# Kernel optimization log

Measured on AMD Instinct MI355X. Metric: run time of the kernel, lower is better.

Reference implementation:

```python
import jax, jax.numpy as jnp
import numpy as np

B, T_V, T_A = 128, 64, 128
E_V, E_A = 1024, 512
H, EMB, C = 1024, 512, 512  # C = input_size - embedding_size
IN = EMB + C               # RNN input size = 1024
VOCAB = 20000


def setup_inputs() -> dict:
    key = jax.random.key(0)
    ks = jax.random.split(key, 26)
    s = 0.02
    inp = {
        "input": jax.random.normal(ks[0], (B, 1, EMB), jnp.float32),
        "enc_visual": jax.random.normal(ks[1], (B, T_V, E_V), jnp.float32),
        "enc_audio": jax.random.normal(ks[2], (B, T_A, E_A), jnp.float32),
        "hidden_state": jax.random.normal(ks[3], (1, B, H), jnp.float32),
        "cell_state": jax.random.normal(ks[4], (1, B, H), jnp.float32),
        # visual attention (Bahdanau): W1:[C,H], W2:[C,E_V], W3:[1,C]
        "W_va1": s * jax.random.normal(ks[5], (C, H), jnp.float32),
        "W_va2": s * jax.random.normal(ks[6], (C, E_V), jnp.float32),
        "W_va3": s * jax.random.normal(ks[7], (1, C), jnp.float32),
        "W_venc": s * jax.random.normal(ks[8], (C, E_V), jnp.float32),
        # audio attention
        "W_aa1": s * jax.random.normal(ks[9], (C, H), jnp.float32),
        "W_aa2": s * jax.random.normal(ks[10], (C, E_A), jnp.float32),
        "W_aa3": s * jax.random.normal(ks[11], (1, C), jnp.float32),
        "W_aenc": s * jax.random.normal(ks[12], (C, E_A), jnp.float32),
        # cross-modal context attention (over 2 context vectors)
        "W_ca1": s * jax.random.normal(ks[13], (C, H), jnp.float32),
        "W_ca2": s * jax.random.normal(ks[14], (C, C), jnp.float32),
        "W_ca3": s * jax.random.normal(ks[15], (1, C), jnp.float32),
        # LSTM-style custom RNN cell params
        "W_ih": s * jax.random.normal(ks[16], (4 * H, IN), jnp.float32),
        "W_hh": s * jax.random.normal(ks[17], (4 * H, H), jnp.float32),
        "b_ih": jnp.zeros((4 * H,), jnp.float32),
        "b_hh": jnp.zeros((4 * H,), jnp.float32),
        # output projection
        "W_out": s * jax.random.normal(ks[18], (VOCAB, H), jnp.float32),
        "b_out": jnp.zeros((VOCAB,), jnp.float32),
    }
    return inp


def _attend(h, enc, W1, W2, W3):
    # h: [B,H]; enc: [B,T,E]. Vectorized Bahdanau attention (original loops over T).
    v1 = h @ W1.T                               # [B,C]
    v2 = jnp.einsum('bte,ce->btc', enc, W2)     # [B,T,C]
    scores = jnp.tanh(v1[:, None, :] + v2) @ W3.T  # [B,T,1]
    attn = jax.nn.softmax(scores[..., 0], axis=1)  # [B,T]
    return jnp.einsum('bt,bte->be', attn, enc)     # [B,E]


def reference(input, enc_visual, enc_audio, hidden_state, cell_state,
              W_va1, W_va2, W_va3, W_venc,
              W_aa1, W_aa2, W_aa3, W_aenc,
              W_ca1, W_ca2, W_ca3,
              W_ih, W_hh, b_ih, b_hh, W_out, b_out):
    h0 = hidden_state[0]   # [B,H]
    c0 = cell_state[0]     # [B,H]

    vc = _attend(h0, enc_visual, W_va1, W_va2, W_va3) @ W_venc.T  # [B,C]
    ac = _attend(h0, enc_audio, W_aa1, W_aa2, W_aa3) @ W_aenc.T   # [B,C]
    all_ctx = jnp.stack([vc, ac], axis=1)                         # [B,2,C]
    final_ctx = _attend(h0, all_ctx, W_ca1, W_ca2, W_ca3)         # [B,C]

    x = jnp.concatenate([input[:, 0, :], jnp.tanh(final_ctx)], axis=-1)  # [B,IN]
    gates = x @ W_ih.T + b_ih + h0 @ W_hh.T + b_hh                 # [B,4H]
    i, f, g, o = jnp.split(gates, 4, axis=-1)
    c_new = jax.nn.sigmoid(f) * c0 + jax.nn.sigmoid(i) * jnp.tanh(g)
    h_new = jax.nn.sigmoid(o) * jnp.tanh(c_new)

    logits = h_new @ W_out.T + b_out                               # [B,V]
    return (logits[:, None, :], h_new[None], c_new[None])
```

## Files before the change

kernel.cpp:

```cpp
#include <hip/hip_runtime.h>
#include <hip/hip_bf16.h>
#include <cstddef>

typedef __attribute__((ext_vector_type(8))) short short8;
typedef __attribute__((ext_vector_type(4))) float f32x4;

static __device__ __forceinline__ f32x4 ldg(const float* p) {
    return *(const f32x4*)p;
}

static __device__ __forceinline__ short8 pack8(f32x4 f0, f32x4 f1) {
    union { __hip_bfloat162 h[4]; short8 s; } u;
    u.h[0] = __float22bfloat162_rn(make_float2(f0.x, f0.y));
    u.h[1] = __float22bfloat162_rn(make_float2(f0.z, f0.w));
    u.h[2] = __float22bfloat162_rn(make_float2(f1.x, f1.y));
    u.h[3] = __float22bfloat162_rn(make_float2(f1.z, f1.w));
    return u.s;
}

static __device__ __forceinline__ void gload16(const short* g, short* l) {
    __builtin_amdgcn_global_load_lds(
        (const __attribute__((address_space(1))) void*)g,
        (__attribute__((address_space(3))) void*)l, 16, 0, 0);
}

static __device__ __forceinline__ void lds_barrier() {
    asm volatile("s_waitcnt lgkmcnt(0)" ::: "memory");
    __builtin_amdgcn_s_barrier();
    asm volatile("" ::: "memory");
}

static __device__ __forceinline__ void sk_body(
    const float* __restrict__ A, int lda,
    const float* __restrict__ W,
    const float* __restrict__ bias, int addbias,
    float* __restrict__ C, int ldc, int N,
    int kbeg, int kend, int n0, int m0)
{
    __shared__ short As[2][128 * 32];
    __shared__ short Ws[2][64 * 32];
    const int tid  = threadIdx.x;
    const int lane = tid & 63;
    const int wave = tid >> 6;
    const int wm = wave * 32;

    f32x4 acc[2][4];
    #pragma unroll
    for (int i = 0; i < 2; ++i)
        #pragma unroll
        for (int j = 0; j < 4; ++j)
            acc[i][j] = (f32x4){0.f, 0.f, 0.f, 0.f};

    const int arow = tid >> 1;
    const int ah   = tid & 1;
    const int afs  = (arow >> 1) & 3;
    const float* gA = A + (size_t)(m0 + arow) * lda + kbeg + ah * 16;
    const int aoff0 = arow * 32 + (((ah * 2)     ^ afs) * 8);
    const int aoff1 = arow * 32 + (((ah * 2 + 1) ^ afs) * 8);

    const int wrow  = tid >> 2;
    const int wslot = tid & 3;
    const int wvalid = (n0 + wrow) < N;
    const float* gW = W + (size_t)(n0 + wrow) * lda + kbeg + wslot * 8;
    const int woff = wrow * 32 + ((wslot ^ ((wrow >> 1) & 3)) * 8);

    const int frow = lane & 15;
    const int hi   = lane >> 4;
    const int fsl  = (hi ^ ((frow >> 1) & 3)) * 8;
    const int ra   = (wm + frow) * 32 + fsl;
    const int rb   = frow * 32 + fsl;

    const int nsteps = (kend - kbeg) >> 5;

    f32x4 a0_[4], a1_[4], w0_[2], w1_[2];
    #pragma unroll
    for (int q = 0; q < 4; ++q) a0_[q] = ldg(gA + q * 4);
    #pragma unroll
    for (int q = 0; q < 4; ++q) a1_[q] = ldg(gA + 32 + q * 4);
    if (wvalid) {
        w0_[0] = ldg(gW);      w0_[1] = ldg(gW + 4);
        w1_[0] = ldg(gW + 32); w1_[1] = ldg(gW + 36);
    } else {
        w0_[0] = w0_[1] = w1_[0] = w1_[1] = (f32x4){0.f, 0.f, 0.f, 0.f};
    }

    for (int s = 0; s < nsteps; s += 2) {
        {
            short* as = As[0]; short* ws = Ws[0];
            *(short8*)(as + aoff0) = pack8(a0_[0], a0_[1]);
            *(short8*)(as + aoff1) = pack8(a0_[2], a0_[3]);
            *(short8*)(ws + woff)  = pack8(w0_[0], w0_[1]);
            if (s + 2 < nsteps) {
                const float* nA = gA + (s + 2) * 32;
                #pragma unroll
                for (int q = 0; q < 4; ++q) a0_[q] = ldg(nA + q * 4);
                if (wvalid) {
                    const float* nW = gW + (s + 2) * 32;
                    w0_[0] = ldg(nW); w0_[1] = ldg(nW + 4);
                }
            }
            lds_barrier();
            short8 af[2], bf[4];
            #pragma unroll
            for (int i = 0; i < 2; ++i) af[i] = *(const short8*)(as + ra + i * 512);
            #pragma unroll
            for (int j = 0; j < 4; ++j) bf[j] = *(const short8*)(ws + rb + j * 512);
            #pragma unroll
            for (int i = 0; i < 2; ++i)
                #pragma unroll
                for (int j = 0; j < 4; ++j)
                    acc[i][j] = __builtin_amdgcn_mfma_f32_16x16x32_bf16(af[i], bf[j], acc[i][j], 0, 0, 0);
        }
        {
            short* as = As[1]; short* ws = Ws[1];
            *(short8*)(as + aoff0) = pack8(a1_[0], a1_[1]);
            *(short8*)(as + aoff1) = pack8(a1_[2], a1_[3]);
            *(short8*)(ws + woff)  = pack8(w1_[0], w1_[1]);
            if (s + 3 < nsteps) {
                const float* nA = gA + (s + 3) * 32;
                #pragma unroll
                for (int q = 0; q < 4; ++q) a1_[q] = ldg(nA + q * 4);
                if (wvalid) {
                    const float* nW = gW + (s + 3) * 32;
                    w1_[0] = ldg(nW); w1_[1] = ldg(nW + 4);
                }
            }
            lds_barrier();
            short8 af[2], bf[4];
            #pragma unroll
            for (int i = 0; i < 2; ++i) af[i] = *(const short8*)(as + ra + i * 512);
            #pragma unroll
            for (int j = 0; j < 4; ++j) bf[j] = *(const short8*)(ws + rb + j * 512);
            #pragma unroll
            for (int i = 0; i < 2; ++i)
                #pragma unroll
                for (int j = 0; j < 4; ++j)
                    acc[i][j] = __builtin_amdgcn_mfma_f32_16x16x32_bf16(af[i], bf[j], acc[i][j], 0, 0, 0);
        }
    }

    const int cl = lane & 15;
    const int rq = hi * 4;
    #pragma unroll
    for (int j = 0; j < 4; ++j) {
        int gc = n0 + j * 16 + cl;
        if (gc >= N) continue;
        float b = addbias ? bias[gc] : 0.f;
        #pragma unroll
        for (int i = 0; i < 2; ++i) {
            int gr = m0 + wm + i * 16 + rq;
            #pragma unroll
            for (int r = 0; r < 4; ++r)
                atomicAdd(C + (size_t)(gr + r) * ldc + gc, acc[i][j][r] + b);
        }
    }
}

__global__ __launch_bounds__(256) void gemm_sk(
    const float* __restrict__ A, const float* __restrict__ W,
    const float* __restrict__ bias, float* __restrict__ C,
    int N, int K, int kchunk, int ldc)
{
    int kbeg = blockIdx.y * kchunk;
    sk_body(A, K, W, bias, bias != nullptr && blockIdx.y == 0,
            C, ldc, N, kbeg, kbeg + kchunk, blockIdx.x * 64, blockIdx.z * 128);
}

__global__ __launch_bounds__(256) void hproj3_mfma(
    const float* __restrict__ h0,
    const float* __restrict__ Wa, const float* __restrict__ Wb, const float* __restrict__ Wc,
    float* __restrict__ hbase)
{
    int n0g = blockIdx.x * 64;
    int wsel = n0g >> 9;
    const float* W = (wsel == 0) ? Wa : (wsel == 1) ? Wb : Wc;
    float* C = hbase + (size_t)wsel * 128 * 512;
    int kbeg = blockIdx.y * 128;
    sk_body(h0, 1024, W, nullptr, 0, C, 512, 512, kbeg, kbeg + 128, n0g & 511, 0);
}

__global__ __launch_bounds__(256) void ctxproj_mfma(
    const float* __restrict__ attv, const float* __restrict__ Wv,
    const float* __restrict__ atta, const float* __restrict__ Wa,
    float* __restrict__ ctx)
{
    const float* A; const float* W; float* C; int lda, kb, ke;
    if (blockIdx.z == 0) { A = attv; W = Wv; C = ctx;       lda = 1024; kb = blockIdx.y * 128; ke = kb + 128; }
    else                 { A = atta; W = Wa; C = ctx + 512; lda = 512;  kb = blockIdx.y * 64;  ke = kb + 64;  }
    sk_body(A, lda, W, nullptr, 0, C, 1024, 512, kb, ke, blockIdx.x * 64, 0);
}

__global__ __launch_bounds__(256) void gates_mfma(
    const float* __restrict__ xb, const float* __restrict__ W_ih,
    const float* __restrict__ h0, const float* __restrict__ W_hh,
    float* __restrict__ gates)
{
    int pair = blockIdx.y >> 2;
    const float* A = pair ? h0 : xb;
    const float* W = pair ? W_hh : W_ih;
    int kb = (blockIdx.y & 3) * 256;
    sk_body(A, 1024, W, nullptr, 0, gates, 4096, 4096, kb, kb + 256, blockIdx.x * 64, 0);
}

__global__ __launch_bounds__(256) void cvt_bf16(
    const float* __restrict__ encv, const float* __restrict__ enca,
    const float* __restrict__ wv2,  const float* __restrict__ wa2,
    short* __restrict__ oev, short* __restrict__ oea,
    short* __restrict__ owv, short* __restrict__ owa)
{
    int bid = blockIdx.x;
    const float* src; short* dst; int lb;
    if (bid < 4096)      { src = encv; dst = oev; lb = bid; }
    else if (bid < 8192) { src = enca; dst = oea; lb = bid - 4096; }
    else if (bid < 8448) { src = wv2;  dst = owv; lb = bid - 8192; }
    else                 { src = wa2;  dst = owa; lb = bid - 8448; }
    size_t off = ((size_t)lb * 256 + threadIdx.x) * 8;
    f32x4 f0 = *(const f32x4*)(src + off);
    f32x4 f1 = *(const f32x4*)(src + off + 4);
    *(short8*)(dst + off) = pack8(f0, f1);
}

__global__ __launch_bounds__(256) void scores_fused(
    const short* __restrict__ Av, const short* __restrict__ Wv,
    const float* __restrict__ hv1,  const float* __restrict__ W_va3,
    float* __restrict__ scv,
    const short* __restrict__ Aa, const short* __restrict__ Wa,
    const float* __restrict__ ha1,  const float* __restrict__ W_aa3,
    float* __restrict__ sca)
{
    __shared__ short As[2][4096];
    __shared__ short Ws[2][4096];

    const short *A, *W; const float *v1, *W3;
    float* sc;
    int K, tshift, n0, m0;
    int idx = blockIdx.x;
    if (idx < 256) {
        n0 = (idx >> 6) * 128;  m0 = (idx & 63) * 128;
        A = Av; W = Wv; v1 = hv1; W3 = W_va3; sc = scv;
        K = 1024; tshift = 6;
    } else {
        idx -= 256;
        n0 = (idx >> 7) * 128;  m0 = (idx & 127) * 128;
        A = Aa; W = Wa; v1 = ha1; W3 = W_aa3; sc = sca;
        K = 512; tshift = 7;
    }

    const int tid  = threadIdx.x;
    const int lane = tid & 63;
    const int wave = tid >> 6;
    const int wr = wave >> 1;
    const int wc = wave & 1;

    f32x4 acc[4][4];
    #pragma unroll
    for (int i = 0; i < 4; ++i)
        #pragma unroll
        for (int j = 0; j < 4; ++j)
            acc[i][j] = (f32x4){0.f, 0.f, 0.f, 0.f};

    const int srow = lane >> 2;
    const int slsw = (lane & 3) ^ ((lane >> 3) & 3);
    const short* gA0 = A + (size_t)(m0 + wave * 16 + srow) * K + slsw * 8;
    const short* gA1 = gA0 + (size_t)64 * K;
    const short* gW0 = W + (size_t)(n0 + wave * 16 + srow) * K + slsw * 8;
    const short* gW1 = gW0 + (size_t)64 * K;
    const int ldsw = wave * 512;

    const int frow = lane & 15;
    const int hi   = lane >> 4;
    const int fsl  = (hi ^ ((frow >> 1) & 3)) * 8;
    const int raBase = (wr * 64 + frow) * 32 + fsl;
    const int rbBase = (wc * 64 + frow) * 32 + fsl;

    const int nsteps = K >> 5;

    gload16(gA0, As[0] + ldsw);
    gload16(gA1, As[0] + 2048 + ldsw);
    gload16(gW0, Ws[0] + ldsw);
    gload16(gW1, Ws[0] + 2048 + ldsw);

    int cur = 0;
    for (int s = 0; s < nsteps; ++s) {
        int nk = (s + 1 < nsteps ? s + 1 : s) * 32;
        gload16(gA0 + nk, As[cur ^ 1] + ldsw);
        gload16(gA1 + nk, As[cur ^ 1] + 2048 + ldsw);
        gload16(gW0 + nk, Ws[cur ^ 1] + ldsw);
        gload16(gW1 + nk, Ws[cur ^ 1] + 2048 + ldsw);
        asm volatile("s_waitcnt vmcnt(4)" ::: "memory");
        __builtin_amdgcn_s_barrier();
        __builtin_amdgcn_sched_barrier(0);

        const short* as = As[cur];
        const short* ws = Ws[cur];
        short8 af[4], bf[4];
        #pragma unroll
        for (int i = 0; i < 4; ++i) af[i] = *(const short8*)(as + raBase + i * 512);
        #pragma unroll
        for (int j = 0; j < 4; ++j) bf[j] = *(const short8*)(ws + rbBase + j * 512);
        #pragma unroll
        for (int i = 0; i < 4; ++i)
            #pragma unroll
            for (int j = 0; j < 4; ++j)
                acc[i][j] = __builtin_amdgcn_mfma_f32_16x16x32_bf16(af[i], bf[j], acc[i][j], 0, 0, 0);
        __builtin_amdgcn_sched_barrier(0);
        __builtin_amdgcn_s_barrier();
        cur ^= 1;
    }

    const int cl = lane & 15;
    const int rq = hi * 4;
    #pragma unroll
    for (int i = 0; i < 4; ++i) {
        #pragma unroll
        for (int r = 0; r < 4; ++r) {
            int gr = m0 + wr * 64 + i * 16 + rq + r;
            const float* v1row = v1 + (size_t)(gr >> tshift) * 512;
            float p = 0.f;
            #pragma unroll
            for (int j = 0; j < 4; ++j) {
                int gc = n0 + wc * 64 + j * 16 + cl;
                p += tanhf(v1row[gc] + acc[i][j][r]) * W3[gc];
            }
            p += __shfl_xor(p, 1, 64);
            p += __shfl_xor(p, 2, 64);
            p += __shfl_xor(p, 4, 64);
            p += __shfl_xor(p, 8, 64);
            if (cl == 0) atomicAdd(sc + gr, p);
        }
    }
}

__global__ __launch_bounds__(256) void attend_out2(
    const float* __restrict__ scv, const float* __restrict__ encv, float* __restrict__ attv,
    const float* __restrict__ sca, const float* __restrict__ enca, float* __restrict__ atta)
{
    const float* sc; const float* enc; float* out;
    int T, E, ec;
    if (blockIdx.y < 4) { sc = scv; enc = encv; out = attv; T = 64;  E = 1024; ec = blockIdx.y; }
    else                { sc = sca; enc = enca; out = atta; T = 128; E = 512;  ec = blockIdx.y - 4; }

    __shared__ float ew[128];
    const int b = blockIdx.x, tid = threadIdx.x;
    __shared__ float raw[128];
    if (tid < T) raw[tid] = sc[(size_t)b * T + tid];
    __syncthreads();
    float m = -1e30f;
    for (int t = 0; t < T; ++t) m = fmaxf(m, raw[t]);
    if (tid < T) ew[tid] = __expf(raw[tid] - m);
    __syncthreads();
    float sum = 0.f;
    for (int t = 0; t < T; ++t) sum += ew[t];
    const float inv = 1.f / sum;

    const int e = ec * 256 + tid;
    const float* encb = enc + (size_t)b * T * E + e;
    float acc = 0.f;
    for (int t = 0; t < T; ++t)
        acc += ew[t] * encb[(size_t)t * E];
    out[(size_t)b * E + e] = acc * inv;
}

__global__ __launch_bounds__(256) void cross_kernel(
    const float* __restrict__ hc1, const float* __restrict__ v2c,
    const float* __restrict__ W3, const float* __restrict__ ctx,
    const float* __restrict__ inp, float* __restrict__ x)
{
    const int C = 512;
    __shared__ float red[256];
    __shared__ float aw[2];
    const int b = blockIdx.x, tid = threadIdx.x;

    float p0 = 0.f, p1 = 0.f;
    for (int c = tid; c < C; c += 256) {
        float h = hc1[(size_t)b * C + c], w = W3[c];
        p0 += tanhf(h + v2c[(size_t)(b * 2 + 0) * C + c]) * w;
        p1 += tanhf(h + v2c[(size_t)(b * 2 + 1) * C + c]) * w;
    }
    red[tid] = p0; __syncthreads();
    for (int s = 128; s; s >>= 1) { if (tid < s) red[tid] += red[tid + s]; __syncthreads(); }
    float s0 = red[0];
    __syncthreads();
    red[tid] = p1; __syncthreads();
    for (int s = 128; s; s >>= 1) { if (tid < s) red[tid] += red[tid + s]; __syncthreads(); }
    if (tid == 0) {
        float s1 = red[0];
        float m = fmaxf(s0, s1);
        float e0 = __expf(s0 - m), e1 = __expf(s1 - m);
        float inv = 1.f / (e0 + e1);
        aw[0] = e0 * inv; aw[1] = e1 * inv;
    }
    __syncthreads();
    float a0 = aw[0], a1 = aw[1];
    for (int c = tid; c < C; c += 256) {
        float fc = a0 * ctx[(size_t)(b * 2 + 0) * C + c]
                 + a1 * ctx[(size_t)(b * 2 + 1) * C + c];
        x[(size_t)b * 1024 + 512 + c] = tanhf(fc);
        x[(size_t)b * 1024 + c] = inp[(size_t)b * 512 + c];
    }
}

__global__ __launch_bounds__(256) void lstm_kernel(
    const float* __restrict__ gates, const float* __restrict__ c0,
    const float* __restrict__ b_ih, const float* __restrict__ b_hh,
    float* __restrict__ hout, float* __restrict__ cout)
{
    const int idx = blockIdx.x * 256 + threadIdx.x;
    const int b = idx >> 10, h = idx & 1023;
    const float* g = gates + (size_t)b * 4096;
    float gi = g[h]        + b_ih[h]        + b_hh[h];
    float gf = g[1024 + h] + b_ih[1024 + h] + b_hh[1024 + h];
    float gg = g[2048 + h] + b_ih[2048 + h] + b_hh[2048 + h];
    float go = g[3072 + h] + b_ih[3072 + h] + b_hh[3072 + h];
    float si = 1.f / (1.f + __expf(-gi));
    float sf = 1.f / (1.f + __expf(-gf));
    float so = 1.f / (1.f + __expf(-go));
    float cn = sf * c0[idx] + si * tanhf(gg);
    float hn = so * tanhf(cn);
    cout[idx] = cn;
    hout[idx] = hn;
}

extern "C" void kernel_launch(void* const* d_in, const int* in_sizes, int n_in,
                              void* d_out, int out_size, void* d_ws, size_t ws_size,
                              hipStream_t stream)
{
    const float* inp    = (const float*)d_in[0];
    const float* encv   = (const float*)d_in[1];
    const float* enca   = (const float*)d_in[2];
    const float* h0     = (const float*)d_in[3];
    const float* c0     = (const float*)d_in[4];
    const float* W_va1  = (const float*)d_in[5];
    const float* W_va2  = (const float*)d_in[6];
    const float* W_va3  = (const float*)d_in[7];
    const float* W_venc = (const float*)d_in[8];
    const float* W_aa1  = (const float*)d_in[9];
    const float* W_aa2  = (const float*)d_in[10];
    const float* W_aa3  = (const float*)d_in[11];
    const float* W_aenc = (const float*)d_in[12];
    const float* W_ca1  = (const float*)d_in[13];
    const float* W_ca2  = (const float*)d_in[14];
    const float* W_ca3  = (const float*)d_in[15];
    const float* W_ih   = (const float*)d_in[16];
    const float* W_hh   = (const float*)d_in[17];
    const float* b_ih   = (const float*)d_in[18];
    const float* b_hh   = (const float*)d_in[19];
    const float* W_out  = (const float*)d_in[20];
    const float* b_out  = (const float*)d_in[21];
    float* out = (float*)d_out;

    float* ws = (float*)d_ws;
    float* hv1  = ws;  ws += 128 * 512;
    float* ha1  = ws;  ws += 128 * 512;
    float* hc1  = ws;  ws += 128 * 512;
    float* scv  = ws;  ws += 128 * 64;
    float* sca  = ws;  ws += 128 * 128;
    float* ctx  = ws;  ws += 128 * 2 * 512;
    float* v2c  = ws;  ws += 128 * 2 * 512;
    float* gates= ws;  ws += (size_t)128 * 4096;
    size_t zero_floats = (size_t)(ws - (float*)d_ws);
    float* xb   = ws;  ws += 128 * 1024;
    float* attv = ws;  ws += 128 * 1024;
    float* atta = ws;  ws += 128 * 512;
    short* encv_bf = (short*)ws;  ws += 8388608 / 2;
    short* enca_bf = (short*)ws;  ws += 8388608 / 2;
    short* wv2_bf  = (short*)ws;  ws += 524288 / 2;
    short* wa2_bf  = (short*)ws;  ws += 262144 / 2;

    dim3 blk(256);

    hipMemsetAsync(d_ws, 0, zero_floats * sizeof(float), stream);
    hipMemsetAsync(out, 0, (size_t)128 * 20000 * sizeof(float), stream);

    cvt_bf16<<<dim3(8576), blk, 0, stream>>>(encv, enca, W_va2, W_aa2,
                                             encv_bf, enca_bf, wv2_bf, wa2_bf);
    hproj3_mfma<<<dim3(24, 8), blk, 0, stream>>>(h0, W_va1, W_aa1, W_ca1, hv1);
    scores_fused<<<dim3(768), blk, 0, stream>>>(encv_bf, wv2_bf, hv1, W_va3, scv,
                                                enca_bf, wa2_bf, ha1, W_aa3, sca);
    attend_out2<<<dim3(128, 6), blk, 0, stream>>>(scv, encv, attv, sca, enca, atta);
    ctxproj_mfma<<<dim3(8, 8, 2), blk, 0, stream>>>(attv, W_venc, atta, W_aenc, ctx);
    gemm_sk<<<dim3(8, 4, 2), blk, 0, stream>>>(ctx, W_ca2, nullptr, v2c, 512, 512, 128, 512);
    cross_kernel<<<128, blk, 0, stream>>>(hc1, v2c, W_ca3, ctx, inp, xb);
    gates_mfma<<<dim3(64, 8), blk, 0, stream>>>(xb, W_ih, h0, W_hh, gates);
    float* hout = out + 2560000;
    float* cout = out + 2560000 + 131072;
    lstm_kernel<<<512, blk, 0, stream>>>(gates, c0, b_ih, b_hh, hout, cout);
    gemm_sk<<<dim3(313, 2, 1), blk, 0, stream>>>(hout, W_out, b_out, out, 20000, 1024, 512, 20000);
}
```

Baseline: 374.6 us.

## Use async global-to-LDS fp32 loads in split-K GEMM and bf16 encoder reads in attention

The split-K GEMM body now stages fp32 A and W tiles directly into LDS with global_load_lds, double-buffered with vmcnt waits. It converts to bf16 while reading fragments from LDS, where before it loaded into registers and packed before storing. Separately, the attention-output kernel reads the bf16 copies of the encoder outputs instead of fp32, halving its traffic and the block count. Risks are higher LDS usage (fp32 tiles), bf16 precision in the weighted sum, and the W row clamping used for out-of-range rows in place of zero fill.

Result: no change. 381.8 us (+1.9%).

```diff
diff --git a/kernel.cpp b/kernel.cpp
--- a/kernel.cpp
+++ b/kernel.cpp
@@ -4,10 +4,6 @@
 
 typedef __attribute__((ext_vector_type(8))) short short8;
 typedef __attribute__((ext_vector_type(4))) float f32x4;
-
-static __device__ __forceinline__ f32x4 ldg(const float* p) {
-    return *(const f32x4*)p;
-}
 
 static __device__ __forceinline__ short8 pack8(f32x4 f0, f32x4 f1) {
     union { __hip_bfloat162 h[4]; short8 s; } u;
@@ -23,11 +19,17 @@
         (const __attribute__((address_space(1))) void*)g,
         (__attribute__((address_space(3))) void*)l, 16, 0, 0);
 }
-
-static __device__ __forceinline__ void lds_barrier() {
-    asm volatile("s_waitcnt lgkmcnt(0)" ::: "memory");
-    __builtin_amdgcn_s_barrier();
-    asm volatile("" ::: "memory");
+static __device__ __forceinline__ void gload16f(const float* g, float* l) {
+    __builtin_amdgcn_global_load_lds(
+        (const __attribute__((address_space(1))) void*)g,
+        (__attribute__((address_space(3))) void*)l, 16, 0, 0);
+}
+
+static __device__ __forceinline__ float bflo(unsigned int u) {
+    union { unsigned int i; float f; } c; c.i = u << 16; return c.f;
+}
+static __device__ __forceinline__ float bfhi(unsigned int u) {
+    union { unsigned int i; float f; } c; c.i = u & 0xffff0000u; return c.f;
 }
 
 static __device__ __forceinline__ void sk_body(
@@ -37,8 +39,8 @@
     float* __restrict__ C, int ldc, int N,
     int kbeg, int kend, int n0, int m0)
 {
-    __shared__ short As[2][128 * 32];
-    __shared__ short Ws[2][64 * 32];
+    __shared__ float As[2][4096];
+    __shared__ float Ws[2][2048];
     const int tid  = threadIdx.x;
     const int lane = tid & 63;
     const int wave = tid >> 6;
@@ -51,92 +53,67 @@
         for (int j = 0; j < 4; ++j)
             acc[i][j] = (f32x4){0.f, 0.f, 0.f, 0.f};
 
-    const int arow = tid >> 1;
-    const int ah   = tid & 1;
-    const int afs  = (arow >> 1) & 3;
-    const float* gA = A + (size_t)(m0 + arow) * lda + kbeg + ah * 16;
-    const int aoff0 = arow * 32 + (((ah * 2)     ^ afs) * 8);
-    const int aoff1 = arow * 32 + (((ah * 2 + 1) ^ afs) * 8);
-
-    const int wrow  = tid >> 2;
-    const int wslot = tid & 3;
-    const int wvalid = (n0 + wrow) < N;
-    const float* gW = W + (size_t)(n0 + wrow) * lda + kbeg + wslot * 8;
-    const int woff = wrow * 32 + ((wslot ^ ((wrow >> 1) & 3)) * 8);
+    const int srow = tid >> 3;
+    const int skof = ((tid >> 2) & 1) * 16 + (((tid & 3) ^ ((tid >> 3) & 3)) * 4);
+    const float* gA = A + (size_t)(m0 + srow) * lda + kbeg + skof;
+    int wr0 = n0 + srow;        if (wr0 > N - 1) wr0 = N - 1;
+    int wr1 = n0 + 32 + srow;   if (wr1 > N - 1) wr1 = N - 1;
+    const float* gW0 = W + (size_t)wr0 * lda + kbeg + skof;
+    const float* gW1 = W + (size_t)wr1 * lda + kbeg + skof;
+    const size_t astep = (size_t)32 * lda;
+    const int ldsw = wave * 256;
 
     const int frow = lane & 15;
     const int hi   = lane >> 4;
-    const int fsl  = (hi ^ ((frow >> 1) & 3)) * 8;
-    const int ra   = (wm + frow) * 32 + fsl;
-    const int rb   = frow * 32 + fsl;
+    const int f3   = frow & 3;
+    const int e1l  = ((2 * (hi & 1))     ^ f3) * 4 + (hi >> 1) * 16;
+    const int e2l  = ((2 * (hi & 1) + 1) ^ f3) * 4 + (hi >> 1) * 16;
+    const int raA  = (wm + frow) * 32;
+    const int raB  = frow * 32;
 
     const int nsteps = (kend - kbeg) >> 5;
 
-    f32x4 a0_[4], a1_[4], w0_[2], w1_[2];
-    #pragma unroll
-    for (int q = 0; q < 4; ++q) a0_[q] = ldg(gA + q * 4);
-    #pragma unroll
-    for (int q = 0; q < 4; ++q) a1_[q] = ldg(gA + 32 + q * 4);
-    if (wvalid) {
-        w0_[0] = ldg(gW);      w0_[1] = ldg(gW + 4);
-        w1_[0] = ldg(gW + 32); w1_[1] = ldg(gW + 36);
-    } else {
-        w0_[0] = w0_[1] = w1_[0] = w1_[1] = (f32x4){0.f, 0.f, 0.f, 0.f};
-    }
-
-    for (int s = 0; s < nsteps; s += 2) {
-        {
-            short* as = As[0]; short* ws = Ws[0];
-            *(short8*)(as + aoff0) = pack8(a0_[0], a0_[1]);
-            *(short8*)(as + aoff1) = pack8(a0_[2], a0_[3]);
-            *(short8*)(ws + woff)  = pack8(w0_[0], w0_[1]);
-            if (s + 2 < nsteps) {
-                const float* nA = gA + (s + 2) * 32;
-                #pragma unroll
-                for (int q = 0; q < 4; ++q) a0_[q] = ldg(nA + q * 4);
-                if (wvalid) {
-                    const float* nW = gW + (s + 2) * 32;
-                    w0_[0] = ldg(nW); w0_[1] = ldg(nW + 4);
-                }
-            }
-            lds_barrier();
-            short8 af[2], bf[4];
+    auto stage = [&](float* asb, float* wsb, int koff) {
+        gload16f(gA + koff,             asb + ldsw);
+        gload16f(gA + astep + koff,     asb + 1024 + ldsw);
+        gload16f(gA + 2 * astep + koff, asb + 2048 + ldsw);
+        gload16f(gA + 3 * astep + koff, asb + 3072 + ldsw);
+        gload16f(gW0 + koff,            wsb + ldsw);
+        gload16f(gW1 + koff,            wsb + 1024 + ldsw);
+    };
+
+    stage(As[0], Ws[0], 0);
+    int cur = 0;
+    for (int s = 0; s < nsteps; ++s) {
+        int nk = (s + 1 < nsteps ? s + 1 : s) * 32;
+        stage(As[cur ^ 1], Ws[cur ^ 1], nk);
+        asm volatile("s_waitcnt vmcnt(6)" ::: "memory");
+        __builtin_amdgcn_s_barrier();
+        __builtin_amdgcn_sched_barrier(0);
+
+        const float* as = As[cur];
+        const float* ws = Ws[cur];
+        short8 af[2], bf[4];
+        #pragma unroll
+        for (int i = 0; i < 2; ++i) {
+            f32x4 lo = *(const f32x4*)(as + raA + i * 512 + e1l);
+            f32x4 hh = *(const f32x4*)(as + raA + i * 512 + e2l);
+            af[i] = pack8(lo, hh);
+        }
+        #pragma unroll
+        for (int j = 0; j < 4; ++j) {
+            f32x4 lo = *(const f32x4*)(ws + raB + j * 512 + e1l);
+            f32x4 hh = *(const f32x4*)(ws + raB + j * 512 + e2l);
+            bf[j] = pack8(lo, hh);
+        }
+        #pragma unroll
+        for (int i = 0; i < 2; ++i)
             #pragma unroll
-            for (int i = 0; i < 2; ++i) af[i] = *(const short8*)(as + ra + i * 512);
-            #pragma unroll
-            for (int j = 0; j < 4; ++j) bf[j] = *(const short8*)(ws + rb + j * 512);
-            #pragma unroll
-            for (int i = 0; i < 2; ++i)
-                #pragma unroll
-                for (int j = 0; j < 4; ++j)
-                    acc[i][j] = __builtin_amdgcn_mfma_f32_16x16x32_bf16(af[i], bf[j], acc[i][j], 0, 0, 0);
-        }
-        {
-            short* as = As[1]; short* ws = Ws[1];
-            *(short8*)(as + aoff0) = pack8(a1_[0], a1_[1]);
-            *(short8*)(as + aoff1) = pack8(a1_[2], a1_[3]);
-            *(short8*)(ws + woff)  = pack8(w1_[0], w1_[1]);
-            if (s + 3 < nsteps) {
-                const float* nA = gA + (s + 3) * 32;
-                #pragma unroll
-                for (int q = 0; q < 4; ++q) a1_[q] = ldg(nA + q * 4);
-                if (wvalid) {
-                    const float* nW = gW + (s + 3) * 32;
-                    w1_[0] = ldg(nW); w1_[1] = ldg(nW + 4);
-                }
-            }
-            lds_barrier();
-            short8 af[2], bf[4];
-            #pragma unroll
-            for (int i = 0; i < 2; ++i) af[i] = *(const short8*)(as + ra + i * 512);
-            #pragma unroll
-            for (int j = 0; j < 4; ++j) bf[j] = *(const short8*)(ws + rb + j * 512);
-            #pragma unroll
-            for (int i = 0; i < 2; ++i)
-                #pragma unroll
-                for (int j = 0; j < 4; ++j)
-                    acc[i][j] = __builtin_amdgcn_mfma_f32_16x16x32_bf16(af[i], bf[j], acc[i][j], 0, 0, 0);
-        }
+            for (int j = 0; j < 4; ++j)
+                acc[i][j] = __builtin_amdgcn_mfma_f32_16x16x32_bf16(af[i], bf[j], acc[i][j], 0, 0, 0);
+        __builtin_amdgcn_sched_barrier(0);
+        __builtin_amdgcn_s_barrier();
+        cur ^= 1;
     }
 
     const int cl = lane & 15;
@@ -332,17 +309,19 @@
 }
 
 __global__ __launch_bounds__(256) void attend_out2(
-    const float* __restrict__ scv, const float* __restrict__ encv, float* __restrict__ attv,
-    const float* __restrict__ sca, const float* __restrict__ enca, float* __restrict__ atta)
-{
-    const float* sc; const float* enc; float* out;
-    int T, E, ec;
-    if (blockIdx.y < 4) { sc = scv; enc = encv; out = attv; T = 64;  E = 1024; ec = blockIdx.y; }
-    else                { sc = sca; enc = enca; out = atta; T = 128; E = 512;  ec = blockIdx.y - 4; }
+    const float* __restrict__ scv, const short* __restrict__ encv_bf, float* __restrict__ attv,
+    const float* __restrict__ sca, const short* __restrict__ enca_bf, float* __restrict__ atta)
+{
+    const float* sc; const unsigned int* enc2; float* out;
+    int T, E2, ec;
+    if (blockIdx.y < 2) { sc = scv; enc2 = (const unsigned int*)encv_bf; out = attv;
+                          T = 64;  E2 = 512; ec = blockIdx.y; }
+    else                { sc = sca; enc2 = (const unsigned int*)enca_bf; out = atta;
+                          T = 128; E2 = 256; ec = 0; }
 
     __shared__ float ew[128];
+    __shared__ float raw[128];
     const int b = blockIdx.x, tid = threadIdx.x;
-    __shared__ float raw[128];
     if (tid < T) raw[tid] = sc[(size_t)b * T + tid];
     __syncthreads();
     float m = -1e30f;
@@ -353,12 +332,17 @@
     for (int t = 0; t < T; ++t) sum += ew[t];
     const float inv = 1.f / sum;
 
-    const int e = ec * 256 + tid;
-    const float* encb = enc + (size_t)b * T * E + e;
-    float acc = 0.f;
-    for (int t = 0; t < T; ++t)
-        acc += ew[t] * encb[(size_t)t * E];
-    out[(size_t)b * E + e] = acc * inv;
+    const int ep = ec * 256 + tid;
+    const unsigned int* encb = enc2 + (size_t)b * T * E2 + ep;
+    float a0 = 0.f, a1 = 0.f;
+    for (int t = 0; t < T; ++t) {
+        unsigned int u = encb[(size_t)t * E2];
+        float w = ew[t];
+        a0 += w * bflo(u);
+        a1 += w * bfhi(u);
+    }
+    out[(size_t)b * E2 * 2 + ep * 2]     = a0 * inv;
+    out[(size_t)b * E2 * 2 + ep * 2 + 1] = a1 * inv;
 }
 
 __global__ __launch_bounds__(256) void cross_kernel(
@@ -477,7 +461,7 @@
     hproj3_mfma<<<dim3(24, 8), blk, 0, stream>>>(h0, W_va1, W_aa1, W_ca1, hv1);
     scores_fused<<<dim3(768), blk, 0, stream>>>(encv_bf, wv2_bf, hv1, W_va3, scv,
                                                 enca_bf, wa2_bf, ha1, W_aa3, sca);
-    attend_out2<<<dim3(128, 6), blk, 0, stream>>>(scv, encv, attv, sca, enca, atta);
+    attend_out2<<<dim3(128, 3), blk, 0, stream>>>(scv, encv_bf, attv, sca, enca_bf, atta);
     ctxproj_mfma<<<dim3(8, 8, 2), blk, 0, stream>>>(attv, W_venc, atta, W_aenc, ctx);
     gemm_sk<<<dim3(8, 4, 2), blk, 0, stream>>>(ctx, W_ca2, nullptr, v2c, 512, 512, 128, 512);
     cross_kernel<<<128, blk, 0, stream>>>(hc1, v2c, W_ca3, ctx, inp, xb);
```
